# Performance work log

Measured on AMD Instinct MI355X. Metric: run time of the kernel, lower is better.

## Reference

```python
import jax, jax.numpy as jnp
import numpy as np

N_NODES = 50000
N_REL = 8
N_EDGES = 60000
F_IN = 128
UNITS = 128


def setup_inputs() -> dict:
    key = jax.random.key(0)
    ks = jax.random.split(key, 7)
    features = jax.random.normal(ks[0], (1, N_NODES, F_IN), dtype=jnp.float32)
    edge_src = jax.random.randint(ks[1], (N_REL, N_EDGES), 0, N_NODES, dtype=jnp.int32)
    edge_dst = jax.random.randint(ks[2], (N_REL, N_EDGES), 0, N_NODES, dtype=jnp.int32)
    edge_w = jax.random.uniform(ks[3], (N_REL, N_EDGES), dtype=jnp.float32)
    scale = 1.0 / np.sqrt(F_IN)
    self_kernel = jax.random.normal(ks[4], (F_IN, UNITS), dtype=jnp.float32) * scale
    rel_kernels = jax.random.normal(ks[5], (N_REL, F_IN, UNITS), dtype=jnp.float32) * scale
    bias = jnp.zeros((UNITS,), dtype=jnp.float32)
    return {"features": features, "edge_src": edge_src, "edge_dst": edge_dst,
            "edge_w": edge_w, "self_kernel": self_kernel,
            "rel_kernels": rel_kernels, "bias": bias}


def reference(features, edge_src, edge_dst, edge_w, self_kernel, rel_kernels, bias):
    # features: [1, N, F]; squeeze the batch dim like the original layer
    x = features[0]                                   # [N, F]
    out = x @ self_kernel                             # [N, U] self-loop term
    # per-relation feature transform: [R, N, U]
    hr = jnp.einsum('nf,rfu->rnu', x, rel_kernels)
    # sparse A_r @ hr via gather at src, weight, segment-sum into dst
    def per_rel(h, s, d, w):
        msg = h[s] * w[:, None]                       # [E, U]
        return jax.ops.segment_sum(msg, d, num_segments=N_NODES)
    agg = jax.vmap(per_rel)(hr, edge_src, edge_dst, edge_w)  # [R, N, U]
    out = out + agg.sum(axis=0) + bias
    out = jax.nn.relu(out)
    return out[None]                                  # [1, N, U]
```

## Files before the change

kernel.cpp:

```cpp
#include <hip/hip_runtime.h>
#include <hip/hip_bf16.h>

#define NN 50000
#define FF 128
#define UU 128
#define NREL 8
#define NE 60000
#define NKEY (NREL * NN)
#define NET (NREL * NE)

typedef __attribute__((ext_vector_type(8))) short bf16x8;
typedef __attribute__((ext_vector_type(4))) float f32x4;


__global__ __launch_bounds__(256) void prepbuild_kernel(
    const float* __restrict__ X, const float* __restrict__ Wself,
    const float* __restrict__ Wrel, const int* __restrict__ esrc,
    const int* __restrict__ edst, const float* __restrict__ ew,
    ushort* __restrict__ Xb, ushort* __restrict__ Wf,
    int* __restrict__ head, int4* __restrict__ rec)
{
    int i = blockIdx.x * 256 + threadIdx.x;
    if (i < NN * FF / 4) {
        float4 v = ((const float4*)X)[i];
        union { __hip_bfloat162 h[2]; uint2 u; } p;
        p.h[0] = __float22bfloat162_rn(make_float2(v.x, v.y));
        p.h[1] = __float22bfloat162_rn(make_float2(v.z, v.w));
        ((uint2*)Xb)[i] = p.u;
    }
    if (i < NET) {
        int key = (i / NE) * NN + edst[i];
        int prev = atomicExch(&head[key], i);
        rec[i] = make_int4(esrc[i], __float_as_int(ew[i]), prev, 0);
    }
    if (i < 9 * FF * UU) {
        int m = i >> 14, k = (i >> 7) & 127, col = i & 127;
        int c = col >> 4, al = col & 15;
        int s = k >> 5, ag = (k >> 3) & 3, j = k & 7;
        float v = (m == 0) ? Wself[i] : Wrel[i - FF * UU];
        __hip_bfloat16 h = __float2bfloat16(v);
        Wf[((m * 8 + c) * 4 + s) * 512 + (ag * 16 + al) * 8 + j] = *(ushort*)&h;
    }
}


#define AGG_L1R(i) int4 r##i = make_int4(0, 0, 0, 0); \
    if (e##i >= 0) r##i = rec[e##i];
#define AGG_L1X(i) uint x##i = 0u; \
    if (e##i >= 0) x##i = *(const uint*)(Xb + (size_t)r##i.x * FF + 2 * l);
#define AGG_L2R(i) int f##i = (e##i >= 0) ? r##i.z : -1; \
    int4 s##i = make_int4(0, 0, 0, 0); \
    if (f##i >= 0) s##i = rec[f##i];
#define AGG_L1A(i) if (e##i >= 0) { \
        float wgt = __int_as_float(r##i.y); \
        ax##i = fmaf(__uint_as_float(x##i << 16), wgt, ax##i); \
        ay##i = fmaf(__uint_as_float(x##i & 0xffff0000u), wgt, ay##i); }
#define AGG_L2X(i) uint y##i = 0u; \
    if (f##i >= 0) y##i = *(const uint*)(Xb + (size_t)s##i.x * FF + 2 * l);
#define AGG_L2A(i) if (f##i >= 0) { \
        float wgt = __int_as_float(s##i.y); \
        ax##i = fmaf(__uint_as_float(y##i << 16), wgt, ax##i); \
        ay##i = fmaf(__uint_as_float(y##i & 0xffff0000u), wgt, ay##i); \
        e##i = s##i.z; \
        if (e##i >= 0) r##i = rec[e##i]; \
    } else e##i = -1;

#define AGG_WALK(e, r, ax, ay)                                              \
    while (e >= 0) {                                                        \
        float w = __int_as_float(r.y);                                      \
        uint x = *(const uint*)(Xb + (size_t)r.x * FF + 2 * l);             \
        e = r.z;                                                            \
        if (e >= 0) r = rec[e];                                             \
        ax = fmaf(__uint_as_float(x << 16), w, ax);                         \
        ay = fmaf(__uint_as_float(x & 0xffff0000u), w, ay);                 \
    }

#define AGG_ST(i) { \
        __hip_bfloat162 hh = __float22bfloat162_rn(make_float2(ax##i, ay##i)); \
        *(uint*)(Zb + (size_t)(k0 + i) * FF + 2 * l) = *(uint*)&hh; }

__global__ __launch_bounds__(256) void agg_kernel(
    const ushort* __restrict__ Xb, const int* __restrict__ head,
    const int4* __restrict__ rec, ushort* __restrict__ Zb)
{
    const int k0 = ((blockIdx.x * 256 + threadIdx.x) >> 6) * 4;
    const int l = threadIdx.x & 63;

    float ax0 = 0.f, ay0 = 0.f, ax1 = 0.f, ay1 = 0.f;
    float ax2 = 0.f, ay2 = 0.f, ax3 = 0.f, ay3 = 0.f;

    const int4 hv = *(const int4*)&head[k0];
    int e0 = hv.x, e1 = hv.y, e2 = hv.z, e3 = hv.w;

    AGG_L1R(0) AGG_L1R(1) AGG_L1R(2) AGG_L1R(3)
    AGG_L1X(0) AGG_L1X(1) AGG_L1X(2) AGG_L1X(3)
    AGG_L2R(0) AGG_L2R(1) AGG_L2R(2) AGG_L2R(3)
    AGG_L1A(0) AGG_L1A(1) AGG_L1A(2) AGG_L1A(3)
    AGG_L2X(0) AGG_L2X(1) AGG_L2X(2) AGG_L2X(3)
    AGG_L2A(0) AGG_L2A(1) AGG_L2A(2) AGG_L2A(3)

    AGG_WALK(e0, r0, ax0, ay0)
    AGG_WALK(e1, r1, ax1, ay1)
    AGG_WALK(e2, r2, ax2, ay2)
    AGG_WALK(e3, r3, ax3, ay3)

    AGG_ST(0) AGG_ST(1) AGG_ST(2) AGG_ST(3)
}


__device__ __forceinline__ void gload_lds16(const uint4* g, uint4* l) {
    __builtin_amdgcn_global_load_lds(
        (const __attribute__((address_space(1))) void*)g,
        (__attribute__((address_space(3))) void*)l, 16, 0, 0);
}

#define LOAD_A(AF, P)                                                        \
    _Pragma("unroll")                                                        \
    for (int s = 0; s < 4; ++s)                                              \
        AF[s] = *(const bf16x8*)((P) + s * 32 + ag * 8);

#define MFMA_BURST(AF)                                                       \
    _Pragma("unroll")                                                        \
    for (int c = 0; c < 8; ++c) {                                            \
        _Pragma("unroll")                                                    \
        for (int s = 0; s < 4; ++s) {                                        \
            bf16x8 bfr = *(const bf16x8*)&bsh[(c * 4 + s) * 64 + l];         \
            acc[c] = __builtin_amdgcn_mfma_f32_16x16x32_bf16(                \
                AF[s], bfr, acc[c], 0, 0, 0);                                \
        }                                                                    \
    }

__global__ __launch_bounds__(256, 4) void gemm_kernel(
    const ushort* __restrict__ Xb, const ushort* __restrict__ Zb,
    const ushort* __restrict__ Wf, const float* __restrict__ bias,
    float* __restrict__ out)
{
    __shared__ uint4 bsh[2048];
    const int t = threadIdx.x;
    const int wid = t >> 6;
    const int l = t & 63;
    const int gw0 = blockIdx.x * 4 + wid;
    const int gwid = (gw0 < NN / 16) ? gw0 : NN / 16 - 1;
    const int R0 = gwid * 16;
    const int al = l & 15;
    const int ag = l >> 4;

    const uint4* Wf4 = (const uint4*)Wf;

    f32x4 acc[8];
    #pragma unroll
    for (int c = 0; c < 8; ++c) acc[c] = (f32x4){0.f, 0.f, 0.f, 0.f};

    bf16x8 aA[4], aB[4];
    {
        const ushort* A0 = Xb + (size_t)(R0 + al) * FF;
        LOAD_A(aA, A0)
    }

    #pragma unroll
    for (int m = 0; m < 9; ++m) {
        __syncthreads();
        {
            const uint4* Wm = Wf4 + m * 2048 + wid * 64 + l;
            uint4* lb = &bsh[wid * 64];
            #pragma unroll
            for (int k = 0; k < 8; ++k)
                gload_lds16(Wm + k * 256, lb + k * 256);
        }
        if (m < 8) {
            const ushort* An = Zb + ((size_t)m * NN + R0 + al) * FF;
            if ((m & 1) == 0) { LOAD_A(aB, An) } else { LOAD_A(aA, An) }
        }
        __syncthreads();
        if ((m & 1) == 0) { MFMA_BURST(aA) } else { MFMA_BURST(aB) }
    }

    #pragma unroll
    for (int c = 0; c < 8; ++c) {
        int col = c * 16 + al;
        float b = bias[col];
        #pragma unroll
        for (int q = 0; q < 4; ++q) {
            int row = R0 + ag * 4 + q;
            out[(size_t)row * UU + col] = fmaxf(acc[c][q] + b, 0.f);
        }
    }
}


extern "C" void kernel_launch(void* const* d_in, const int* in_sizes, int n_in,
                              void* d_out, int out_size, void* d_ws, size_t ws_size,
                              hipStream_t stream) {
    const float* X     = (const float*)d_in[0];
    const int*   esrc  = (const int*)d_in[1];
    const int*   edst  = (const int*)d_in[2];
    const float* ew    = (const float*)d_in[3];
    const float* Wself = (const float*)d_in[4];
    const float* Wrel  = (const float*)d_in[5];
    const float* bias  = (const float*)d_in[6];
    float* out = (float*)d_out;

    ushort* Zb   = (ushort*)d_ws;
    ushort* Xb   = Zb + (size_t)NKEY * FF;
    ushort* Wf   = Xb + (size_t)NN * FF;
    int*    head = (int*)(Wf + 9 * FF * UU);
    int4*   rec  = (int4*)(head + NKEY);

    hipMemsetAsync(head, 0xFF, NKEY * sizeof(int), stream);
    hipLaunchKernelGGL(prepbuild_kernel, dim3(NN * FF / 4 / 256), dim3(256), 0, stream,
                       X, Wself, Wrel, esrc, edst, ew, Xb, Wf, head, rec);
    hipLaunchKernelGGL(agg_kernel,  dim3(NKEY / 16), dim3(256), 0, stream,
                       Xb, head, rec, Zb);
    hipLaunchKernelGGL(gemm_kernel, dim3((NN / 16 + 3) / 4), dim3(256), 0, stream,
                       Xb, Zb, Wf, bias, out);
}
```

Baseline: 123.6 us.

## Pipeline GEMM weight staging with quad-buffered LDS half-tiles and manual waitcnt

The GEMM loop is split into 18 half-steps, each covering 64 output columns of one weight matrix. Weight half-tiles are staged into a 4-slot LDS ring two steps ahead via global_load_lds, and A fragments are triple-buffered. Explicit s_waitcnt vmcnt plus a raw s_barrier replace the two __syncthreads per matrix, so loads overlap MFMA work instead of stalling each iteration. LDS doubles to 64KB and launch bounds drop to 2 blocks per CU, which lowers occupancy. The hand-counted vmcnt values risk subtle races if the compiler reorders memory ops.

```diff
diff --git a/kernel.cpp b/kernel.cpp
--- a/kernel.cpp
+++ b/kernel.cpp
@@ -114,28 +114,36 @@
         (__attribute__((address_space(3))) void*)l, 16, 0, 0);
 }
 
+#define STAGE_H(q) { \
+        const uint4* Ws = Wf4 + ((q) >> 1) * 2048 + ((q) & 1) * 1024 + wid * 64 + l; \
+        uint4* lb = &bsh[((q) & 3) * 1024 + wid * 64]; \
+        _Pragma("unroll") \
+        for (int k = 0; k < 4; ++k) \
+            gload_lds16(Ws + k * 256, lb + k * 256); }
+
 #define LOAD_A(AF, P)                                                        \
     _Pragma("unroll")                                                        \
     for (int s = 0; s < 4; ++s)                                              \
         AF[s] = *(const bf16x8*)((P) + s * 32 + ag * 8);
 
-#define MFMA_BURST(AF)                                                       \
+#define HBURST(AF, p)                                                        \
     _Pragma("unroll")                                                        \
-    for (int c = 0; c < 8; ++c) {                                            \
+    for (int cl = 0; cl < 4; ++cl) {                                         \
         _Pragma("unroll")                                                    \
         for (int s = 0; s < 4; ++s) {                                        \
-            bf16x8 bfr = *(const bf16x8*)&bsh[(c * 4 + s) * 64 + l];         \
-            acc[c] = __builtin_amdgcn_mfma_f32_16x16x32_bf16(                \
-                AF[s], bfr, acc[c], 0, 0, 0);                                \
+            bf16x8 bfr = *(const bf16x8*)&bsh[((p) & 3) * 1024 +             \
+                                              (cl * 4 + s) * 64 + l];        \
+            acc[((p) & 1) * 4 + cl] = __builtin_amdgcn_mfma_f32_16x16x32_bf16( \
+                AF[s], bfr, acc[((p) & 1) * 4 + cl], 0, 0, 0);               \
         }                                                                    \
     }
 
-__global__ __launch_bounds__(256, 4) void gemm_kernel(
+__global__ __launch_bounds__(256, 2) void gemm_kernel(
     const ushort* __restrict__ Xb, const ushort* __restrict__ Zb,
     const ushort* __restrict__ Wf, const float* __restrict__ bias,
     float* __restrict__ out)
 {
-    __shared__ uint4 bsh[2048];
+    __shared__ uint4 bsh[4 * 1024];
     const int t = threadIdx.x;
     const int wid = t >> 6;
     const int l = t & 63;
@@ -144,6 +152,7 @@
     const int R0 = gwid * 16;
     const int al = l & 15;
     const int ag = l >> 4;
+    const int arow = R0 + al;
 
     const uint4* Wf4 = (const uint4*)Wf;
 
@@ -151,28 +160,31 @@
     #pragma unroll
     for (int c = 0; c < 8; ++c) acc[c] = (f32x4){0.f, 0.f, 0.f, 0.f};
 
-    bf16x8 aA[4], aB[4];
-    {
-        const ushort* A0 = Xb + (size_t)(R0 + al) * FF;
-        LOAD_A(aA, A0)
-    }
+    bf16x8 aX[4], aY[4], aZ[4];
+    LOAD_A(aX, Xb + (size_t)arow * FF)
+    STAGE_H(0)
+    STAGE_H(1)
 
     #pragma unroll
-    for (int m = 0; m < 9; ++m) {
-        __syncthreads();
+    for (int p = 0; p < 18; ++p) {
+        if (p < 16) STAGE_H(p + 2)
+        if ((p & 1) == 0 && p <= 14) {
+            const int j = p / 2 + 1;
+            const ushort* An = Zb + ((size_t)(j - 1) * NN + arow) * FF;
+            if (j % 3 == 0)      { LOAD_A(aX, An) }
+            else if (j % 3 == 1) { LOAD_A(aY, An) }
+            else                 { LOAD_A(aZ, An) }
+        }
+        if (p < 16)       { asm volatile("s_waitcnt vmcnt(12)" ::: "memory"); }
+        else if (p == 16) { asm volatile("s_waitcnt vmcnt(4)"  ::: "memory"); }
+        else              { asm volatile("s_waitcnt vmcnt(0)"  ::: "memory"); }
+        __builtin_amdgcn_s_barrier();
         {
-            const uint4* Wm = Wf4 + m * 2048 + wid * 64 + l;
-            uint4* lb = &bsh[wid * 64];
-            #pragma unroll
-            for (int k = 0; k < 8; ++k)
-                gload_lds16(Wm + k * 256, lb + k * 256);
+            const int j = p >> 1;
+            if (j % 3 == 0)      { HBURST(aX, p) }
+            else if (j % 3 == 1) { HBURST(aY, p) }
+            else                 { HBURST(aZ, p) }
         }
-        if (m < 8) {
-            const ushort* An = Zb + ((size_t)m * NN + R0 + al) * FF;
-            if ((m & 1) == 0) { LOAD_A(aB, An) } else { LOAD_A(aA, An) }
-        }
-        __syncthreads();
-        if ((m & 1) == 0) { MFMA_BURST(aA) } else { MFMA_BURST(aB) }
     }
 
     #pragma unroll
```

After: 154.4 us. +24.9%, slower.
